# Kernel tuning notes

Hardware: AMD Instinct MI355X
Metric: run time of the kernel (lower is better)

The kernel has to match this reference:

```python
import jax, jax.numpy as jnp
import numpy as np

D_MODEL = 1024
NUM_HEADS = 16
DEPTH = D_MODEL // NUM_HEADS
NEG_BIG = -1e9


def setup_inputs() -> dict:
    key = jax.random.key(0)
    ks = jax.random.split(key, 12)
    B, S = 2, 2048
    scale = 1.0 / np.sqrt(D_MODEL)
    inp = {
        "v": jax.random.normal(ks[0], (B, S, D_MODEL), jnp.float32),
        "k": jax.random.normal(ks[1], (B, S, D_MODEL), jnp.float32),
        "q": jax.random.normal(ks[2], (B, S, D_MODEL), jnp.float32),
        "mask": jnp.zeros((B, 1, 1, S), jnp.float32),
        "Wq": jax.random.normal(ks[3], (D_MODEL, D_MODEL), jnp.float32) * scale,
        "bq": jnp.zeros((D_MODEL,), jnp.float32),
        "Wk": jax.random.normal(ks[4], (D_MODEL, D_MODEL), jnp.float32) * scale,
        "bk": jnp.zeros((D_MODEL,), jnp.float32),
        "Wv": jax.random.normal(ks[5], (D_MODEL, D_MODEL), jnp.float32) * scale,
        "bv": jnp.zeros((D_MODEL,), jnp.float32),
        "Wo": jax.random.normal(ks[6], (D_MODEL, D_MODEL), jnp.float32) * scale,
        "bo": jnp.zeros((D_MODEL,), jnp.float32),
    }
    return inp


def _split_heads(x):
    # (B, S, D) -> (B, H, S, depth)
    B, S, _ = x.shape
    return x.reshape(B, S, NUM_HEADS, DEPTH).transpose(0, 2, 1, 3)


def reference(v, k, q, mask, Wq, bq, Wk, bk, Wv, bv, Wo, bo):
    B, S, _ = q.shape
    qh = _split_heads(q @ Wq + bq)  # (B,H,Sq,depth)
    kh = _split_heads(k @ Wk + bk)  # (B,H,Sk,depth)
    vh = _split_heads(v @ Wv + bv)  # (B,H,Sk,depth)

    logits = jnp.einsum("bhqd,bhkd->bhqk", qh, kh) / jnp.sqrt(
        jnp.asarray(DEPTH, jnp.float32))
    logits = logits + mask * NEG_BIG  # mask broadcasts over heads/queries
    attn = jax.nn.softmax(logits, axis=-1)  # (B,H,Sq,Sk)
    ctx = jnp.einsum("bhqk,bhkd->bhqd", attn, vh)
    ctx = ctx.transpose(0, 2, 1, 3).reshape(B, S, D_MODEL)
    out = ctx @ Wo + bo
    return out, attn
```

## Files before the change

### kernel.cpp

```cpp
#include <hip/hip_runtime.h>
#include <stdint.h>

#define S_LEN 2048
#define DMODEL 1024
#define NHEAD 16
#define DHEAD 64
#define NBATCH 2
#define NE 4194304
#define WN 1048576

typedef unsigned short u16;
typedef float f32x16 __attribute__((ext_vector_type(16)));
typedef __bf16 bf16x8 __attribute__((ext_vector_type(8)));

__device__ __forceinline__ u16 f2bf(float x) {
  union { float f; unsigned u; } v; v.f = x;
  unsigned r = v.u + 0x7fffu + ((v.u >> 16) & 1u);
  return (u16)(r >> 16);
}
__device__ __forceinline__ unsigned cvt_pk_bf16(float lo, float hi) {
  unsigned r;
  asm("v_cvt_pk_bf16_f32 %0, %1, %2" : "=v"(r) : "v"(lo), "v"(hi));
  return r;
}
__device__ __forceinline__ void gld_lds16(const void* g, void* l) {
  __builtin_amdgcn_global_load_lds(
      (const __attribute__((address_space(1))) unsigned*)g,
      (__attribute__((address_space(3))) unsigned*)l, 16, 0, 0);
}

__global__ __launch_bounds__(256) void cvt_inputs(
    const float* __restrict__ q, const float* __restrict__ k, const float* __restrict__ v,
    u16* __restrict__ xq, u16* __restrict__ xk, u16* __restrict__ xv)
{
  int i = blockIdx.x * 256 + threadIdx.x;
  const int stride = gridDim.x * 256;
  for (; i < NE / 4; i += stride) {
    float4 a = ((const float4*)q)[i];
    float4 b = ((const float4*)k)[i];
    float4 c = ((const float4*)v)[i];
    ushort4 oa, ob, oc;
    oa.x = f2bf(a.x); oa.y = f2bf(a.y); oa.z = f2bf(a.z); oa.w = f2bf(a.w);
    ob.x = f2bf(b.x); ob.y = f2bf(b.y); ob.z = f2bf(b.z); ob.w = f2bf(b.w);
    oc.x = f2bf(c.x); oc.y = f2bf(c.y); oc.z = f2bf(c.z); oc.w = f2bf(c.w);
    ((ushort4*)xq)[i] = oa;
    ((ushort4*)xk)[i] = ob;
    ((ushort4*)xv)[i] = oc;
  }
}

__global__ __launch_bounds__(256) void wtrans(
    const float* __restrict__ Wq, const float* __restrict__ Wk,
    const float* __restrict__ Wv, const float* __restrict__ Wo,
    u16* __restrict__ oq, u16* __restrict__ ok, u16* __restrict__ ov, u16* __restrict__ oo)
{
  __shared__ u16 t[64][65];
  const float* W; u16* O;
  if (blockIdx.z == 0)      { W = Wq; O = oq; }
  else if (blockIdx.z == 1) { W = Wk; O = ok; }
  else if (blockIdx.z == 2) { W = Wv; O = ov; }
  else                      { W = Wo; O = oo; }
  const int tid = threadIdx.x;
  const int r0 = blockIdx.y * 64, c0 = blockIdx.x * 64;
#pragma unroll
  for (int i = 0; i < 4; ++i) {
    const int row = i * 16 + (tid >> 4);
    const int col = (tid & 15) * 4;
    float4 wv = *(const float4*)(W + (size_t)(r0 + row) * DMODEL + c0 + col);
    t[row][col + 0] = f2bf(wv.x);
    t[row][col + 1] = f2bf(wv.y);
    t[row][col + 2] = f2bf(wv.z);
    t[row][col + 3] = f2bf(wv.w);
  }
  __syncthreads();
#pragma unroll
  for (int i = 0; i < 4; ++i) {
    const int row = i * 16 + (tid >> 4);
    const int col = (tid & 15) * 4;
    ushort4 o;
    o.x = t[col + 0][row]; o.y = t[col + 1][row];
    o.z = t[col + 2][row]; o.w = t[col + 3][row];
    *(ushort4*)(O + (size_t)(c0 + row) * DMODEL + r0 + col) = o;
  }
}

template <int OUTMODE>
__device__ __forceinline__ void gemm_core(
    const u16* __restrict__ A, const u16* __restrict__ Bt,
    const float* __restrict__ bias, void* __restrict__ outp,
    float scale, int m0, int n0)
{
  __shared__ u16 As[128 * 32];
  __shared__ u16 Bs[128 * 32];
  const int tid = threadIdx.x;
  const int lane = tid & 63, w = tid >> 6;
  const int q_l = lane & 31, hi = lane >> 5;
  const int wr = w >> 1, wc = w & 1;

  f32x16 acc[2][2];
#pragma unroll
  for (int a = 0; a < 2; ++a)
#pragma unroll
    for (int b = 0; b < 2; ++b)
#pragma unroll
      for (int r = 0; r < 16; ++r) acc[a][b][r] = 0.f;

  const u16* srcA = A + (size_t)(m0 + (tid >> 2)) * DMODEL + (tid & 3) * 8;
  const u16* srcB = Bt + (size_t)(n0 + (tid >> 2)) * DMODEL + (tid & 3) * 8;
  u16* dstA = As + w * 512;
  u16* dstB = Bs + w * 512;

  for (int kt = 0; kt < DMODEL; kt += 32) {
    gld_lds16(srcA + kt, dstA);
    gld_lds16(srcA + kt + (size_t)64 * DMODEL, dstA + 2048);
    gld_lds16(srcB + kt, dstB);
    gld_lds16(srcB + kt + (size_t)64 * DMODEL, dstB + 2048);
    __syncthreads();
#pragma unroll
    for (int kk = 0; kk < 2; ++kk) {
      bf16x8 af[2], bfv[2];
#pragma unroll
      for (int mb = 0; mb < 2; ++mb)
        af[mb] = *reinterpret_cast<const bf16x8*>(&As[(wr * 64 + mb * 32 + q_l) * 32 + kk * 16 + hi * 8]);
#pragma unroll
      for (int nb = 0; nb < 2; ++nb)
        bfv[nb] = *reinterpret_cast<const bf16x8*>(&Bs[(wc * 64 + nb * 32 + q_l) * 32 + kk * 16 + hi * 8]);
#pragma unroll
      for (int mb = 0; mb < 2; ++mb)
#pragma unroll
        for (int nb = 0; nb < 2; ++nb)
          acc[mb][nb] = __builtin_amdgcn_mfma_f32_32x32x16_bf16(af[mb], bfv[nb], acc[mb][nb], 0, 0, 0);
    }
    __syncthreads();
  }

#pragma unroll
  for (int mb = 0; mb < 2; ++mb) {
#pragma unroll
    for (int nb = 0; nb < 2; ++nb) {
      const int n = n0 + wc * 64 + nb * 32 + q_l;
      const float bn = bias[n];
#pragma unroll
      for (int r = 0; r < 16; ++r) {
        const int m = m0 + wr * 64 + mb * 32 + (r & 3) + 8 * (r >> 2) + 4 * hi;
        const float val = (acc[mb][nb][r] + bn) * scale;
        if (OUTMODE == 0) {
          const int bb = m >> 11, s = m & 2047, hh = n >> 6, d = n & 63;
          ((u16*)outp)[(((size_t)(bb * NHEAD + hh)) * S_LEN + s) * DHEAD + d] = f2bf(val);
        } else {
          ((float*)outp)[(size_t)m * DMODEL + n] = val;
        }
      }
    }
  }
}

__global__ __launch_bounds__(256) void gemm_qkv(
    const u16* __restrict__ xq, const u16* __restrict__ xk, const u16* __restrict__ xv,
    const u16* __restrict__ wqt, const u16* __restrict__ wkt, const u16* __restrict__ wvt,
    const float* __restrict__ bq, const float* __restrict__ bk, const float* __restrict__ bv,
    u16* __restrict__ qh, u16* __restrict__ kh, u16* __restrict__ vh)
{
  const u16 *A, *Bt; const float* bias; u16* O; float scale;
  if (blockIdx.z == 0)      { A = xq; Bt = wqt; bias = bq; O = qh; scale = 0.125f; }
  else if (blockIdx.z == 1) { A = xk; Bt = wkt; bias = bk; O = kh; scale = 1.f; }
  else                      { A = xv; Bt = wvt; bias = bv; O = vh; scale = 1.f; }
  gemm_core<0>(A, Bt, bias, O, scale, blockIdx.y * 128, blockIdx.x * 128);
}

__global__ __launch_bounds__(256) void vtrans(const u16* __restrict__ vh, u16* __restrict__ vt)
{
  __shared__ u16 t[64][72];
  const int tid = threadIdx.x;
  const int id = blockIdx.x;
  const int h = ((id & 7) << 1) | ((id >> 3) & 1);
  const int b = (id >> 4) & 1;
  const int bh = b * 16 + h;
  const int s0 = (id >> 5) * 64;
  const u16* src = vh + (size_t)bh * S_LEN * DHEAD;
  u16* dst = vt + (size_t)bh * DHEAD * S_LEN;
#pragma unroll
  for (int i = 0; i < 2; ++i) {
    const int row = i * 32 + (tid >> 3);
    const int c8 = (tid & 7) * 8;
    *(uint4*)&t[row][c8] = *(const uint4*)(src + (size_t)(s0 + row) * DHEAD + c8);
  }
  __syncthreads();
#pragma unroll
  for (int i = 0; i < 2; ++i) {
    const int d = i * 32 + (tid >> 3);
    const int c8 = (tid & 7) * 8;
    unsigned p0 = (unsigned)t[c8 + 0][d] | ((unsigned)t[c8 + 1][d] << 16);
    unsigned p1 = (unsigned)t[c8 + 2][d] | ((unsigned)t[c8 + 3][d] << 16);
    unsigned p2 = (unsigned)t[c8 + 4][d] | ((unsigned)t[c8 + 5][d] << 16);
    unsigned p3 = (unsigned)t[c8 + 6][d] | ((unsigned)t[c8 + 7][d] << 16);
    uint4 o; o.x = p0; o.y = p1; o.z = p2; o.w = p3;
    *(uint4*)(dst + (size_t)d * S_LEN + s0 + c8) = o;
  }
}

__global__ __launch_bounds__(64) void attn_pv(
    const u16* __restrict__ qh, const u16* __restrict__ kh,
    const u16* __restrict__ vt, const float* __restrict__ mask,
    float* __restrict__ inv_g, u16* __restrict__ ctx_out)
{
  const int lane = threadIdx.x;
  const int q_l = lane & 31, hi = lane >> 5;
  const int id = blockIdx.x;
  const int h = ((id & 7) << 1) | ((id >> 3) & 1);
  const int b = (id >> 4) & 1;
  const int bh = b * 16 + h;
  const int qb = id >> 5;
  const int q0 = qb * 32;

  const u16* Qp = qh + (size_t)bh * S_LEN * DHEAD;
  const u16* Kp = kh + (size_t)bh * S_LEN * DHEAD;
  const u16* Vp = vt + (size_t)bh * DHEAD * S_LEN;
  const float* mrow = mask + (size_t)b * S_LEN;

  bf16x8 qf[4];
  {
    const u16* qrow = Qp + (size_t)(q0 + q_l) * DHEAD + hi * 8;
#pragma unroll
    for (int c = 0; c < 4; ++c) qf[c] = *reinterpret_cast<const bf16x8*>(qrow + c * 16);
  }

  float rsum = 0.f;
  f32x16 cacc[2];
#pragma unroll
  for (int db = 0; db < 2; ++db)
#pragma unroll
    for (int r = 0; r < 16; ++r) cacc[db][r] = 0.f;

  bf16x8 kc[4], kn[4], vc[2][2], vn[2][2];
  {
    const u16* kr0 = Kp + (size_t)q_l * DHEAD + hi * 8;
#pragma unroll
    for (int c = 0; c < 4; ++c) kc[c] = *reinterpret_cast<const bf16x8*>(kr0 + c * 16);
#pragma unroll
    for (int s2 = 0; s2 < 2; ++s2)
#pragma unroll
      for (int db = 0; db < 2; ++db)
        vc[s2][db] = *reinterpret_cast<const bf16x8*>(
            Vp + (size_t)(db * 32 + q_l) * S_LEN + s2 * 16 + hi * 8);
  }

#pragma unroll 2
  for (int t = 0; t < 64; ++t) {
    const int k0 = t * 32;
    if (t < 63) {
      const u16* krow = Kp + (size_t)(k0 + 32 + q_l) * DHEAD + hi * 8;
#pragma unroll
      for (int c = 0; c < 4; ++c) kn[c] = *reinterpret_cast<const bf16x8*>(krow + c * 16);
#pragma unroll
      for (int s2 = 0; s2 < 2; ++s2)
#pragma unroll
        for (int db = 0; db < 2; ++db)
          vn[s2][db] = *reinterpret_cast<const bf16x8*>(
              Vp + (size_t)(db * 32 + q_l) * S_LEN + k0 + 32 + s2 * 16 + hi * 8);
    }
    f32x16 a0, a1;
#pragma unroll
    for (int r = 0; r < 16; ++r) { a0[r] = 0.f; a1[r] = 0.f; }
    a0 = __builtin_amdgcn_mfma_f32_32x32x16_bf16(kc[0], qf[0], a0, 0, 0, 0);
    a0 = __builtin_amdgcn_mfma_f32_32x32x16_bf16(kc[1], qf[1], a0, 0, 0, 0);
    a1 = __builtin_amdgcn_mfma_f32_32x32x16_bf16(kc[2], qf[2], a1, 0, 0, 0);
    a1 = __builtin_amdgcn_mfma_f32_32x32x16_bf16(kc[3], qf[3], a1, 0, 0, 0);

    float p[16];
#pragma unroll
    for (int g = 0; g < 4; ++g) {
      const float4 mk = *(const float4*)&mrow[k0 + 8 * g + 4 * hi];
      p[4 * g + 0] = __expf(a0[4 * g + 0] + a1[4 * g + 0] + mk.x * -1e9f);
      p[4 * g + 1] = __expf(a0[4 * g + 1] + a1[4 * g + 1] + mk.y * -1e9f);
      p[4 * g + 2] = __expf(a0[4 * g + 2] + a1[4 * g + 2] + mk.z * -1e9f);
      p[4 * g + 3] = __expf(a0[4 * g + 3] + a1[4 * g + 3] + mk.w * -1e9f);
      rsum += (p[4 * g + 0] + p[4 * g + 1]) + (p[4 * g + 2] + p[4 * g + 3]);
    }
    unsigned pk[8];
#pragma unroll
    for (int g = 0; g < 4; ++g) {
      pk[2 * g + 0] = cvt_pk_bf16(p[4 * g + 0], p[4 * g + 1]);
      pk[2 * g + 1] = cvt_pk_bf16(p[4 * g + 2], p[4 * g + 3]);
    }
#pragma unroll
    for (int s2 = 0; s2 < 2; ++s2) {
      unsigned a0u = pk[4 * s2 + 0], b0u = pk[4 * s2 + 2];
      unsigned a1u = pk[4 * s2 + 1], b1u = pk[4 * s2 + 3];
      asm volatile("v_permlane32_swap_b32 %0, %1" : "+v"(a0u), "+v"(b0u));
      asm volatile("v_permlane32_swap_b32 %0, %1" : "+v"(a1u), "+v"(b1u));
      uint4 frw; frw.x = a0u; frw.y = a1u; frw.z = b0u; frw.w = b1u;
      bf16x8 pa = __builtin_bit_cast(bf16x8, frw);
#pragma unroll
      for (int db = 0; db < 2; ++db)
        cacc[db] = __builtin_amdgcn_mfma_f32_32x32x16_bf16(pa, vc[s2][db], cacc[db], 0, 0, 0);
    }
#pragma unroll
    for (int c = 0; c < 4; ++c) kc[c] = kn[c];
#pragma unroll
    for (int s2 = 0; s2 < 2; ++s2)
#pragma unroll
      for (int db = 0; db < 2; ++db) vc[s2][db] = vn[s2][db];
  }

  rsum += __shfl_xor(rsum, 32, 64);
  const float inv = 1.0f / rsum;
  if (lane < 32) inv_g[(size_t)bh * S_LEN + q0 + lane] = inv;

  float sc[16];
#pragma unroll
  for (int r = 0; r < 16; ++r)
    sc[r] = __shfl(inv, (r & 3) + 8 * (r >> 2) + 4 * hi, 64);
#pragma unroll
  for (int db = 0; db < 2; ++db)
#pragma unroll
    for (int r = 0; r < 16; ++r) {
      const int qq = (r & 3) + 8 * (r >> 2) + 4 * hi;
      ctx_out[((size_t)(b * S_LEN + q0 + qq)) * DMODEL + h * DHEAD + db * 32 + q_l] =
          f2bf(cacc[db][r] * sc[r]);
    }
}

__global__ __launch_bounds__(256) void tail_fused(
    const u16* __restrict__ ctx, const u16* __restrict__ wot, const float* __restrict__ bo,
    float* __restrict__ out,
    const u16* __restrict__ qh, const u16* __restrict__ kh,
    const float* __restrict__ mask, const float* __restrict__ inv_g,
    float* __restrict__ attn_out)
{
  if (blockIdx.x < 256) {
    const int gid = blockIdx.x;
    gemm_core<1>(ctx, wot, bo, out, 1.f, (gid >> 3) * 128, (gid & 7) * 128);
    return;
  }
  const int id = blockIdx.x - 256;
  const int tid = threadIdx.x;
  const int lane = tid & 63, w = tid >> 6;
  const int q_l = lane & 31, hi = lane >> 5;
  const int h = ((id & 7) << 1) | ((id >> 3) & 1);
  const int b = (id >> 4) & 1;
  const int bh = b * 16 + h;
  const int qb = id >> 5;
  const int q0 = qb * 32;

  const u16* Qp = qh + (size_t)bh * S_LEN * DHEAD;
  const u16* Kp = kh + (size_t)bh * S_LEN * DHEAD;

  bf16x8 qf[4];
  {
    const u16* qrow = Qp + (size_t)(q0 + q_l) * DHEAD + hi * 8;
#pragma unroll
    for (int c = 0; c < 4; ++c) qf[c] = *reinterpret_cast<const bf16x8*>(qrow + c * 16);
  }

  float myinv[16];
#pragma unroll
  for (int r = 0; r < 16; ++r)
    myinv[r] = inv_g[(size_t)bh * S_LEN + q0 + (r & 3) + 8 * (r >> 2) + 4 * hi];

  const int k0w = w * 512;
  float mval[16];
#pragma unroll
  for (int t = 0; t < 16; ++t)
    mval[t] = mask[(size_t)b * S_LEN + k0w + t * 32 + q_l] * -1e9f;

  float* base = attn_out + ((size_t)bh * S_LEN + q0 + 4 * hi) * S_LEN + k0w + q_l;

  bf16x8 kc[4], kn[4];
  {
    const u16* kr0 = Kp + (size_t)(k0w + q_l) * DHEAD + hi * 8;
#pragma unroll
    for (int c = 0; c < 4; ++c) kc[c] = *reinterpret_cast<const bf16x8*>(kr0 + c * 16);
  }

#pragma unroll
  for (int t = 0; t < 16; ++t) {
    if (t < 15) {
      const u16* krow = Kp + (size_t)(k0w + (t + 1) * 32 + q_l) * DHEAD + hi * 8;
#pragma unroll
      for (int c = 0; c < 4; ++c) kn[c] = *reinterpret_cast<const bf16x8*>(krow + c * 16);
    }
    f32x16 a0, a1;
#pragma unroll
    for (int r = 0; r < 16; ++r) { a0[r] = 0.f; a1[r] = 0.f; }
    a0 = __builtin_amdgcn_mfma_f32_32x32x16_bf16(qf[0], kc[0], a0, 0, 0, 0);
    a0 = __builtin_amdgcn_mfma_f32_32x32x16_bf16(qf[1], kc[1], a0, 0, 0, 0);
    a1 = __builtin_amdgcn_mfma_f32_32x32x16_bf16(qf[2], kc[2], a1, 0, 0, 0);
    a1 = __builtin_amdgcn_mfma_f32_32x32x16_bf16(qf[3], kc[3], a1, 0, 0, 0);
#pragma unroll
    for (int r = 0; r < 16; ++r) {
      const float pv = __expf(a0[r] + a1[r] + mval[t]) * myinv[r];
      const int rr = (r & 3) + 8 * (r >> 2);
      __builtin_nontemporal_store(pv, &base[(size_t)rr * S_LEN + t * 32]);
    }
#pragma unroll
    for (int c = 0; c < 4; ++c) kc[c] = kn[c];
  }
}

extern "C" void kernel_launch(void* const* d_in, const int* in_sizes, int n_in,
                              void* d_out, int out_size, void* d_ws, size_t ws_size,
                              hipStream_t stream)
{
  (void)in_sizes; (void)n_in; (void)out_size; (void)ws_size;
  const float* v    = (const float*)d_in[0];
  const float* k    = (const float*)d_in[1];
  const float* q    = (const float*)d_in[2];
  const float* mask = (const float*)d_in[3];
  const float* Wq   = (const float*)d_in[4];
  const float* bq   = (const float*)d_in[5];
  const float* Wk   = (const float*)d_in[6];
  const float* bk   = (const float*)d_in[7];
  const float* Wv   = (const float*)d_in[8];
  const float* bv   = (const float*)d_in[9];
  const float* Wo   = (const float*)d_in[10];
  const float* bo   = (const float*)d_in[11];

  u16* ws16 = (u16*)d_ws;
  u16* xq  = ws16;
  u16* xk  = ws16 + (size_t)1 * NE;
  u16* xv  = ws16 + (size_t)2 * NE;
  u16* qh  = ws16 + (size_t)3 * NE;
  u16* kh  = ws16 + (size_t)4 * NE;
  u16* vh  = ws16 + (size_t)5 * NE;
  u16* wqt = ws16 + (size_t)6 * NE;
  u16* wkt = wqt + WN;
  u16* wvt = wkt + WN;
  u16* wot = wvt + WN;
  float* inv_g = (float*)(wot + WN);
  u16* vt  = xq;
  u16* ctx = xk;

  float* outp  = (float*)d_out;
  float* attnp = outp + (size_t)NE;

  cvt_inputs<<<dim3(1024), dim3(256), 0, stream>>>(q, k, v, xq, xk, xv);
  wtrans<<<dim3(16, 16, 4), dim3(256), 0, stream>>>(Wq, Wk, Wv, Wo, wqt, wkt, wvt, wot);
  gemm_qkv<<<dim3(8, 32, 3), dim3(256), 0, stream>>>(xq, xk, xv, wqt, wkt, wvt,
                                                     bq, bk, bv, qh, kh, vh);
  vtrans<<<dim3(1024), dim3(256), 0, stream>>>(vh, vt);
  attn_pv<<<dim3(2048), dim3(64), 0, stream>>>(qh, kh, vt, mask, inv_g, ctx);
  tail_fused<<<dim3(2304), dim3(256), 0, stream>>>(ctx, wot, bo, outp,
                                                   qh, kh, mask, inv_g, attnp);
}
```

Before: 314.1 us.

## Run PV and attention-probability writing concurrently in one kernel, split output GEMM

Merges the PV/context computation and the attention-matrix writer into one launch with 2560 blocks, so the memory-bound attn write overlaps the compute-bound PV pass. The attn writer no longer waits on a global inv_g buffer; instead each block recomputes the row sums itself across 4 waves and reduces them in shared memory. The output projection GEMM moves to its own kernel after the mega kernel. The cost is a redundant QK^T and exp pass for the row sums in the writer blocks, plus the PV path now packs 4 waves per block.

```diff
diff --git a/kernel.cpp b/kernel.cpp
--- a/kernel.cpp
+++ b/kernel.cpp
@@ -168,6 +168,13 @@
   gemm_core<0>(A, Bt, bias, O, scale, blockIdx.y * 128, blockIdx.x * 128);
 }
 
+__global__ __launch_bounds__(256) void gemm_out(
+    const u16* __restrict__ ctx, const u16* __restrict__ wot,
+    const float* __restrict__ bo, float* __restrict__ out)
+{
+  gemm_core<1>(ctx, wot, bo, out, 1.f, blockIdx.y * 128, blockIdx.x * 128);
+}
+
 __global__ __launch_bounds__(256) void vtrans(const u16* __restrict__ vh, u16* __restrict__ vt)
 {
   __shared__ u16 t[64][72];
@@ -199,23 +206,142 @@
   }
 }
 
-__global__ __launch_bounds__(64) void attn_pv(
+__global__ __launch_bounds__(256) void attn_mega(
     const u16* __restrict__ qh, const u16* __restrict__ kh,
     const u16* __restrict__ vt, const float* __restrict__ mask,
-    float* __restrict__ inv_g, u16* __restrict__ ctx_out)
-{
-  const int lane = threadIdx.x;
+    u16* __restrict__ ctx_out, float* __restrict__ attn_out)
+{
+  const int tid = threadIdx.x;
+  const int lane = tid & 63, w = tid >> 6;
   const int q_l = lane & 31, hi = lane >> 5;
-  const int id = blockIdx.x;
+
+  if (blockIdx.x < 512) {
+    const int ib = blockIdx.x;
+    const int x = ib & 7;
+    const int j = ((ib >> 3) << 2) + w;
+    const int h = (x << 1) | (j & 1);
+    const int b = (j >> 1) & 1;
+    const int bh = b * 16 + h;
+    const int q0 = (j >> 2) * 32;
+
+    const u16* Qp = qh + (size_t)bh * S_LEN * DHEAD;
+    const u16* Kp = kh + (size_t)bh * S_LEN * DHEAD;
+    const u16* Vp = vt + (size_t)bh * DHEAD * S_LEN;
+    const float* mrow = mask + (size_t)b * S_LEN;
+
+    bf16x8 qf[4];
+    {
+      const u16* qrow = Qp + (size_t)(q0 + q_l) * DHEAD + hi * 8;
+#pragma unroll
+      for (int c = 0; c < 4; ++c) qf[c] = *reinterpret_cast<const bf16x8*>(qrow + c * 16);
+    }
+
+    float rsum = 0.f;
+    f32x16 cacc[2];
+#pragma unroll
+    for (int db = 0; db < 2; ++db)
+#pragma unroll
+      for (int r = 0; r < 16; ++r) cacc[db][r] = 0.f;
+
+    bf16x8 kc[4], kn[4], vc[2][2], vn[2][2];
+    {
+      const u16* kr0 = Kp + (size_t)q_l * DHEAD + hi * 8;
+#pragma unroll
+      for (int c = 0; c < 4; ++c) kc[c] = *reinterpret_cast<const bf16x8*>(kr0 + c * 16);
+#pragma unroll
+      for (int s2 = 0; s2 < 2; ++s2)
+#pragma unroll
+        for (int db = 0; db < 2; ++db)
+          vc[s2][db] = *reinterpret_cast<const bf16x8*>(
+              Vp + (size_t)(db * 32 + q_l) * S_LEN + s2 * 16 + hi * 8);
+    }
+
+#pragma unroll 2
+    for (int t = 0; t < 64; ++t) {
+      const int k0 = t * 32;
+      if (t < 63) {
+        const u16* krow = Kp + (size_t)(k0 + 32 + q_l) * DHEAD + hi * 8;
+#pragma unroll
+        for (int c = 0; c < 4; ++c) kn[c] = *reinterpret_cast<const bf16x8*>(krow + c * 16);
+#pragma unroll
+        for (int s2 = 0; s2 < 2; ++s2)
+#pragma unroll
+          for (int db = 0; db < 2; ++db)
+            vn[s2][db] = *reinterpret_cast<const bf16x8*>(
+                Vp + (size_t)(db * 32 + q_l) * S_LEN + k0 + 32 + s2 * 16 + hi * 8);
+      }
+      f32x16 a0, a1;
+#pragma unroll
+      for (int r = 0; r < 16; ++r) { a0[r] = 0.f; a1[r] = 0.f; }
+      a0 = __builtin_amdgcn_mfma_f32_32x32x16_bf16(kc[0], qf[0], a0, 0, 0, 0);
+      a0 = __builtin_amdgcn_mfma_f32_32x32x16_bf16(kc[1], qf[1], a0, 0, 0, 0);
+      a1 = __builtin_amdgcn_mfma_f32_32x32x16_bf16(kc[2], qf[2], a1, 0, 0, 0);
+      a1 = __builtin_amdgcn_mfma_f32_32x32x16_bf16(kc[3], qf[3], a1, 0, 0, 0);
+
+      float p[16];
+#pragma unroll
+      for (int g = 0; g < 4; ++g) {
+        const float4 mk = *(const float4*)&mrow[k0 + 8 * g + 4 * hi];
+        p[4 * g + 0] = __expf(a0[4 * g + 0] + a1[4 * g + 0] + mk.x * -1e9f);
+        p[4 * g + 1] = __expf(a0[4 * g + 1] + a1[4 * g + 1] + mk.y * -1e9f);
+        p[4 * g + 2] = __expf(a0[4 * g + 2] + a1[4 * g + 2] + mk.z * -1e9f);
+        p[4 * g + 3] = __expf(a0[4 * g + 3] + a1[4 * g + 3] + mk.w * -1e9f);
+        rsum += (p[4 * g + 0] + p[4 * g + 1]) + (p[4 * g + 2] + p[4 * g + 3]);
+      }
+      unsigned pk[8];
+#pragma unroll
+      for (int g = 0; g < 4; ++g) {
+        pk[2 * g + 0] = cvt_pk_bf16(p[4 * g + 0], p[4 * g + 1]);
+        pk[2 * g + 1] = cvt_pk_bf16(p[4 * g + 2], p[4 * g + 3]);
+      }
+#pragma unroll
+      for (int s2 = 0; s2 < 2; ++s2) {
+        unsigned a0u = pk[4 * s2 + 0], b0u = pk[4 * s2 + 2];
+        unsigned a1u = pk[4 * s2 + 1], b1u = pk[4 * s2 + 3];
+        asm volatile("v_permlane32_swap_b32 %0, %1" : "+v"(a0u), "+v"(b0u));
+        asm volatile("v_permlane32_swap_b32 %0, %1" : "+v"(a1u), "+v"(b1u));
+        uint4 frw; frw.x = a0u; frw.y = a1u; frw.z = b0u; frw.w = b1u;
+        bf16x8 pa = __builtin_bit_cast(bf16x8, frw);
+#pragma unroll
+        for (int db = 0; db < 2; ++db)
+          cacc[db] = __builtin_amdgcn_mfma_f32_32x32x16_bf16(pa, vc[s2][db], cacc[db], 0, 0, 0);
+      }
+#pragma unroll
+      for (int c = 0; c < 4; ++c) kc[c] = kn[c];
+#pragma unroll
+      for (int s2 = 0; s2 < 2; ++s2)
+#pragma unroll
+        for (int db = 0; db < 2; ++db) vc[s2][db] = vn[s2][db];
+    }
+
+    rsum += __shfl_xor(rsum, 32, 64);
+    const float inv = 1.0f / rsum;
+    float sc[16];
+#pragma unroll
+    for (int r = 0; r < 16; ++r)
+      sc[r] = __shfl(inv, (r & 3) + 8 * (r >> 2) + 4 * hi, 64);
+#pragma unroll
+    for (int db = 0; db < 2; ++db)
+#pragma unroll
+      for (int r = 0; r < 16; ++r) {
+        const int qq = (r & 3) + 8 * (r >> 2) + 4 * hi;
+        ctx_out[((size_t)(b * S_LEN + q0 + qq)) * DMODEL + h * DHEAD + db * 32 + q_l] =
+            f2bf(cacc[db][r] * sc[r]);
+      }
+    return;
+  }
+
+  __shared__ float srow[4][32];
+  __shared__ float sinv[32];
+  const int id = blockIdx.x - 512;
   const int h = ((id & 7) << 1) | ((id >> 3) & 1);
   const int b = (id >> 4) & 1;
   const int bh = b * 16 + h;
-  const int qb = id >> 5;
-  const int q0 = qb * 32;
+  const int q0 = (id >> 5) * 32;
+  const int k0w = w * 512;
 
   const u16* Qp = qh + (size_t)bh * S_LEN * DHEAD;
   const u16* Kp = kh + (size_t)bh * S_LEN * DHEAD;
-  const u16* Vp = vt + (size_t)bh * DHEAD * S_LEN;
   const float* mrow = mask + (size_t)b * S_LEN;
 
   bf16x8 qf[4];
@@ -226,143 +352,54 @@
   }
 
   float rsum = 0.f;
-  f32x16 cacc[2];
-#pragma unroll
-  for (int db = 0; db < 2; ++db)
-#pragma unroll
-    for (int r = 0; r < 16; ++r) cacc[db][r] = 0.f;
-
-  bf16x8 kc[4], kn[4], vc[2][2], vn[2][2];
   {
-    const u16* kr0 = Kp + (size_t)q_l * DHEAD + hi * 8;
+    bf16x8 kc[4], kn[4];
+    const u16* kr0 = Kp + (size_t)(k0w + q_l) * DHEAD + hi * 8;
 #pragma unroll
     for (int c = 0; c < 4; ++c) kc[c] = *reinterpret_cast<const bf16x8*>(kr0 + c * 16);
 #pragma unroll
-    for (int s2 = 0; s2 < 2; ++s2)
-#pragma unroll
-      for (int db = 0; db < 2; ++db)
-        vc[s2][db] = *reinterpret_cast<const bf16x8*>(
-            Vp + (size_t)(db * 32 + q_l) * S_LEN + s2 * 16 + hi * 8);
-  }
-
-#pragma unroll 2
-  for (int t = 0; t < 64; ++t) {
-    const int k0 = t * 32;
-    if (t < 63) {
-      const u16* krow = Kp + (size_t)(k0 + 32 + q_l) * DHEAD + hi * 8;
-#pragma unroll
-      for (int c = 0; c < 4; ++c) kn[c] = *reinterpret_cast<const bf16x8*>(krow + c * 16);
-#pragma unroll
-      for (int s2 = 0; s2 < 2; ++s2)
-#pragma unroll
-        for (int db = 0; db < 2; ++db)
-          vn[s2][db] = *reinterpret_cast<const bf16x8*>(
-              Vp + (size_t)(db * 32 + q_l) * S_LEN + k0 + 32 + s2 * 16 + hi * 8);
-    }
-    f32x16 a0, a1;
-#pragma unroll
-    for (int r = 0; r < 16; ++r) { a0[r] = 0.f; a1[r] = 0.f; }
-    a0 = __builtin_amdgcn_mfma_f32_32x32x16_bf16(kc[0], qf[0], a0, 0, 0, 0);
-    a0 = __builtin_amdgcn_mfma_f32_32x32x16_bf16(kc[1], qf[1], a0, 0, 0, 0);
-    a1 = __builtin_amdgcn_mfma_f32_32x32x16_bf16(kc[2], qf[2], a1, 0, 0, 0);
-    a1 = __builtin_amdgcn_mfma_f32_32x32x16_bf16(kc[3], qf[3], a1, 0, 0, 0);
-
-    float p[16];
-#pragma unroll
-    for (int g = 0; g < 4; ++g) {
-      const float4 mk = *(const float4*)&mrow[k0 + 8 * g + 4 * hi];
-      p[4 * g + 0] = __expf(a0[4 * g + 0] + a1[4 * g + 0] + mk.x * -1e9f);
-      p[4 * g + 1] = __expf(a0[4 * g + 1] + a1[4 * g + 1] + mk.y * -1e9f);
-      p[4 * g + 2] = __expf(a0[4 * g + 2] + a1[4 * g + 2] + mk.z * -1e9f);
-      p[4 * g + 3] = __expf(a0[4 * g + 3] + a1[4 * g + 3] + mk.w * -1e9f);
-      rsum += (p[4 * g + 0] + p[4 * g + 1]) + (p[4 * g + 2] + p[4 * g + 3]);
-    }
-    unsigned pk[8];
-#pragma unroll
-    for (int g = 0; g < 4; ++g) {
-      pk[2 * g + 0] = cvt_pk_bf16(p[4 * g + 0], p[4 * g + 1]);
-      pk[2 * g + 1] = cvt_pk_bf16(p[4 * g + 2], p[4 * g + 3]);
-    }
-#pragma unroll
-    for (int s2 = 0; s2 < 2; ++s2) {
-      unsigned a0u = pk[4 * s2 + 0], b0u = pk[4 * s2 + 2];
-      unsigned a1u = pk[4 * s2 + 1], b1u = pk[4 * s2 + 3];
-      asm volatile("v_permlane32_swap_b32 %0, %1" : "+v"(a0u), "+v"(b0u));
-      asm volatile("v_permlane32_swap_b32 %0, %1" : "+v"(a1u), "+v"(b1u));
-      uint4 frw; frw.x = a0u; frw.y = a1u; frw.z = b0u; frw.w = b1u;
-      bf16x8 pa = __builtin_bit_cast(bf16x8, frw);
-#pragma unroll
-      for (int db = 0; db < 2; ++db)
-        cacc[db] = __builtin_amdgcn_mfma_f32_32x32x16_bf16(pa, vc[s2][db], cacc[db], 0, 0, 0);
-    }
-#pragma unroll
-    for (int c = 0; c < 4; ++c) kc[c] = kn[c];
-#pragma unroll
-    for (int s2 = 0; s2 < 2; ++s2)
-#pragma unroll
-      for (int db = 0; db < 2; ++db) vc[s2][db] = vn[s2][db];
-  }
-
+    for (int t = 0; t < 16; ++t) {
+      const int k0 = k0w + t * 32;
+      if (t < 15) {
+        const u16* krow = Kp + (size_t)(k0 + 32 + q_l) * DHEAD + hi * 8;
+#pragma unroll
+        for (int c = 0; c < 4; ++c) kn[c] = *reinterpret_cast<const bf16x8*>(krow + c * 16);
+      }
+      f32x16 a0, a1;
+#pragma unroll
+      for (int r = 0; r < 16; ++r) { a0[r] = 0.f; a1[r] = 0.f; }
+      a0 = __builtin_amdgcn_mfma_f32_32x32x16_bf16(kc[0], qf[0], a0, 0, 0, 0);
+      a0 = __builtin_amdgcn_mfma_f32_32x32x16_bf16(kc[1], qf[1], a0, 0, 0, 0);
+      a1 = __builtin_amdgcn_mfma_f32_32x32x16_bf16(kc[2], qf[2], a1, 0, 0, 0);
+      a1 = __builtin_amdgcn_mfma_f32_32x32x16_bf16(kc[3], qf[3], a1, 0, 0, 0);
+#pragma unroll
+      for (int g = 0; g < 4; ++g) {
+        const float4 mk = *(const float4*)&mrow[k0 + 8 * g + 4 * hi];
+        rsum += __expf(a0[4 * g + 0] + a1[4 * g + 0] + mk.x * -1e9f)
+              + __expf(a0[4 * g + 1] + a1[4 * g + 1] + mk.y * -1e9f)
+              + __expf(a0[4 * g + 2] + a1[4 * g + 2] + mk.z * -1e9f)
+              + __expf(a0[4 * g + 3] + a1[4 * g + 3] + mk.w * -1e9f);
+      }
+#pragma unroll
+      for (int c = 0; c < 4; ++c) kc[c] = kn[c];
+    }
+  }
   rsum += __shfl_xor(rsum, 32, 64);
-  const float inv = 1.0f / rsum;
-  if (lane < 32) inv_g[(size_t)bh * S_LEN + q0 + lane] = inv;
-
-  float sc[16];
+  if (lane < 32) srow[w][q_l] = rsum;
+  __syncthreads();
+  if (tid < 32)
+    sinv[tid] = 1.0f / (srow[0][tid] + srow[1][tid] + srow[2][tid] + srow[3][tid]);
+  __syncthreads();
+
+  float myinv[16];
 #pragma unroll
   for (int r = 0; r < 16; ++r)
-    sc[r] = __shfl(inv, (r & 3) + 8 * (r >> 2) + 4 * hi, 64);
-#pragma unroll
-  for (int db = 0; db < 2; ++db)
-#pragma unroll
-    for (int r = 0; r < 16; ++r) {
-      const int qq = (r & 3) + 8 * (r >> 2) + 4 * hi;
-      ctx_out[((size_t)(b * S_LEN + q0 + qq)) * DMODEL + h * DHEAD + db * 32 + q_l] =
-          f2bf(cacc[db][r] * sc[r]);
-    }
-}
-
-__global__ __launch_bounds__(256) void tail_fused(
-    const u16* __restrict__ ctx, const u16* __restrict__ wot, const float* __restrict__ bo,
-    float* __restrict__ out,
-    const u16* __restrict__ qh, const u16* __restrict__ kh,
-    const float* __restrict__ mask, const float* __restrict__ inv_g,
-    float* __restrict__ attn_out)
-{
-  if (blockIdx.x < 256) {
-    const int gid = blockIdx.x;
-    gemm_core<1>(ctx, wot, bo, out, 1.f, (gid >> 3) * 128, (gid & 7) * 128);
-    return;
-  }
-  const int id = blockIdx.x - 256;
-  const int tid = threadIdx.x;
-  const int lane = tid & 63, w = tid >> 6;
-  const int q_l = lane & 31, hi = lane >> 5;
-  const int h = ((id & 7) << 1) | ((id >> 3) & 1);
-  const int b = (id >> 4) & 1;
-  const int bh = b * 16 + h;
-  const int qb = id >> 5;
-  const int q0 = qb * 32;
-
-  const u16* Qp = qh + (size_t)bh * S_LEN * DHEAD;
-  const u16* Kp = kh + (size_t)bh * S_LEN * DHEAD;
-
-  bf16x8 qf[4];
-  {
-    const u16* qrow = Qp + (size_t)(q0 + q_l) * DHEAD + hi * 8;
-#pragma unroll
-    for (int c = 0; c < 4; ++c) qf[c] = *reinterpret_cast<const bf16x8*>(qrow + c * 16);
-  }
-
-  float myinv[16];
-#pragma unroll
-  for (int r = 0; r < 16; ++r)
-    myinv[r] = inv_g[(size_t)bh * S_LEN + q0 + (r & 3) + 8 * (r >> 2) + 4 * hi];
-
-  const int k0w = w * 512;
+    myinv[r] = sinv[(r & 3) + 8 * (r >> 2) + 4 * hi];
+
   float mval[16];
 #pragma unroll
   for (int t = 0; t < 16; ++t)
-    mval[t] = mask[(size_t)b * S_LEN + k0w + t * 32 + q_l] * -1e9f;
+    mval[t] = mrow[k0w + t * 32 + q_l] * -1e9f;
 
   float* base = attn_out + ((size_t)bh * S_LEN + q0 + 4 * hi) * S_LEN + k0w + q_l;
 
@@ -427,7 +464,6 @@
   u16* wkt = wqt + WN;
   u16* wvt = wkt + WN;
   u16* wot = wvt + WN;
-  float* inv_g = (float*)(wot + WN);
   u16* vt  = xq;
   u16* ctx = xk;
 
@@ -439,7 +475,6 @@
   gemm_qkv<<<dim3(8, 32, 3), dim3(256), 0, stream>>>(xq, xk, xv, wqt, wkt, wvt,
                                                      bq, bk, bv, qh, kh, vh);
   vtrans<<<dim3(1024), dim3(256), 0, stream>>>(vh, vt);
-  attn_pv<<<dim3(2048), dim3(64), 0, stream>>>(qh, kh, vt, mask, inv_g, ctx);
-  tail_fused<<<dim3(2304), dim3(256), 0, stream>>>(ctx, wot, bo, outp,
-                                                   qh, kh, mask, inv_g, attnp);
-}
+  attn_mega<<<dim3(2560), dim3(256), 0, stream>>>(qh, kh, vt, mask, ctx, attnp);
+  gemm_out<<<dim3(8, 32), dim3(256), 0, stream>>>(ctx, wot, bo, outp);
+}
```

After: 379.3 us. 1.21x slower.

## Split attention key loop across two waves with shared-memory reduction

Applied to the files above, without the earlier changes.

The attention kernel now runs two wavefronts per block, each covering half of the key sequence (32 tiles instead of 64). Partial row sums and context accumulators go to shared memory, are added after a barrier, normalized, and written as vectorized 16-element bf16 stores. This is meant to halve the serial loop length per wave and add parallelism. In exchange it adds LDS use (about 16KB per block), a sync and a reduction step.

```diff
diff --git a/kernel.cpp b/kernel.cpp
--- a/kernel.cpp
+++ b/kernel.cpp
@@ -199,12 +199,16 @@
   }
 }
 
-__global__ __launch_bounds__(64) void attn_pv(
+__global__ __launch_bounds__(128) void attn_pv(
     const u16* __restrict__ qh, const u16* __restrict__ kh,
     const u16* __restrict__ vt, const float* __restrict__ mask,
     float* __restrict__ inv_g, u16* __restrict__ ctx_out)
 {
-  const int lane = threadIdx.x;
+  __shared__ float sred[2][32][64];
+  __shared__ float srow[2][32];
+
+  const int tid = threadIdx.x;
+  const int lane = tid & 63, w = tid >> 6;
   const int q_l = lane & 31, hi = lane >> 5;
   const int id = blockIdx.x;
   const int h = ((id & 7) << 1) | ((id >> 3) & 1);
@@ -232,9 +236,11 @@
 #pragma unroll
     for (int r = 0; r < 16; ++r) cacc[db][r] = 0.f;
 
+  const int tb = w * 32;
+
   bf16x8 kc[4], kn[4], vc[2][2], vn[2][2];
   {
-    const u16* kr0 = Kp + (size_t)q_l * DHEAD + hi * 8;
+    const u16* kr0 = Kp + (size_t)(tb * 32 + q_l) * DHEAD + hi * 8;
 #pragma unroll
     for (int c = 0; c < 4; ++c) kc[c] = *reinterpret_cast<const bf16x8*>(kr0 + c * 16);
 #pragma unroll
@@ -242,13 +248,13 @@
 #pragma unroll
       for (int db = 0; db < 2; ++db)
         vc[s2][db] = *reinterpret_cast<const bf16x8*>(
-            Vp + (size_t)(db * 32 + q_l) * S_LEN + s2 * 16 + hi * 8);
+            Vp + (size_t)(db * 32 + q_l) * S_LEN + tb * 32 + s2 * 16 + hi * 8);
   }
 
 #pragma unroll 2
-  for (int t = 0; t < 64; ++t) {
-    const int k0 = t * 32;
-    if (t < 63) {
+  for (int t = 0; t < 32; ++t) {
+    const int k0 = (tb + t) * 32;
+    if (t < 31) {
       const u16* krow = Kp + (size_t)(k0 + 32 + q_l) * DHEAD + hi * 8;
 #pragma unroll
       for (int c = 0; c < 4; ++c) kn[c] = *reinterpret_cast<const bf16x8*>(krow + c * 16);
@@ -304,21 +310,31 @@
   }
 
   rsum += __shfl_xor(rsum, 32, 64);
-  const float inv = 1.0f / rsum;
-  if (lane < 32) inv_g[(size_t)bh * S_LEN + q0 + lane] = inv;
-
-  float sc[16];
-#pragma unroll
-  for (int r = 0; r < 16; ++r)
-    sc[r] = __shfl(inv, (r & 3) + 8 * (r >> 2) + 4 * hi, 64);
+  if (lane < 32) srow[w][lane] = rsum;
 #pragma unroll
   for (int db = 0; db < 2; ++db)
 #pragma unroll
     for (int r = 0; r < 16; ++r) {
       const int qq = (r & 3) + 8 * (r >> 2) + 4 * hi;
-      ctx_out[((size_t)(b * S_LEN + q0 + qq)) * DMODEL + h * DHEAD + db * 32 + q_l] =
-          f2bf(cacc[db][r] * sc[r]);
-    }
+      sred[w][qq][db * 32 + q_l] = cacc[db][r];
+    }
+  __syncthreads();
+
+  if (tid < 32)
+    inv_g[(size_t)bh * S_LEN + q0 + tid] = 1.0f / (srow[0][tid] + srow[1][tid]);
+
+  {
+    const int row = tid >> 2;
+    const int d0 = (tid & 3) * 16;
+    const float inv = 1.0f / (srow[0][row] + srow[1][row]);
+    union { u16 us[16]; uint4 v[2]; } ou;
+#pragma unroll
+    for (int j = 0; j < 16; ++j)
+      ou.us[j] = f2bf((sred[0][row][d0 + j] + sred[1][row][d0 + j]) * inv);
+    u16* base = ctx_out + ((size_t)(b * S_LEN + q0 + row)) * DMODEL + h * DHEAD + d0;
+    *(uint4*)base = ou.v[0];
+    *(uint4*)(base + 8) = ou.v[1];
+  }
 }
 
 __global__ __launch_bounds__(256) void tail_fused(
@@ -439,7 +455,7 @@
   gemm_qkv<<<dim3(8, 32, 3), dim3(256), 0, stream>>>(xq, xk, xv, wqt, wkt, wvt,
                                                      bq, bk, bv, qh, kh, vh);
   vtrans<<<dim3(1024), dim3(256), 0, stream>>>(vh, vt);
-  attn_pv<<<dim3(2048), dim3(64), 0, stream>>>(qh, kh, vt, mask, inv_g, ctx);
+  attn_pv<<<dim3(2048), dim3(128), 0, stream>>>(qh, kh, vt, mask, inv_g, ctx);
   tail_fused<<<dim3(2304), dim3(256), 0, stream>>>(ctx, wot, bo, outp,
                                                    qh, kh, mask, inv_g, attnp);
 }
```

Result: no change. 316.0 us (+0.6%).

## Process two 32-query tiles per block to reuse K/V loads

Applied to the files above, without the earlier changes.

Each attn_pv and tail_fused block now handles 64 queries as two 32-row sub-tiles that share the same K and V fragment loads, halving grid sizes. This cuts global/L2 traffic for K and V per query and amortises the loop and mask overhead. In exchange it raises register pressure (double accumulators and Q fragments), lowers the unroll to 1, and leaves fewer blocks, which reduces occupancy and parallelism.

```diff
diff --git a/kernel.cpp b/kernel.cpp
--- a/kernel.cpp
+++ b/kernel.cpp
@@ -199,7 +199,7 @@
   }
 }
 
-__global__ __launch_bounds__(64) void attn_pv(
+__global__ __launch_bounds__(64, 2) void attn_pv(
     const u16* __restrict__ qh, const u16* __restrict__ kh,
     const u16* __restrict__ vt, const float* __restrict__ mask,
     float* __restrict__ inv_g, u16* __restrict__ ctx_out)
@@ -211,26 +211,30 @@
   const int b = (id >> 4) & 1;
   const int bh = b * 16 + h;
   const int qb = id >> 5;
-  const int q0 = qb * 32;
+  const int q0 = qb * 64;
 
   const u16* Qp = qh + (size_t)bh * S_LEN * DHEAD;
   const u16* Kp = kh + (size_t)bh * S_LEN * DHEAD;
   const u16* Vp = vt + (size_t)bh * DHEAD * S_LEN;
   const float* mrow = mask + (size_t)b * S_LEN;
 
-  bf16x8 qf[4];
+  bf16x8 qfA[4], qfB[4];
   {
-    const u16* qrow = Qp + (size_t)(q0 + q_l) * DHEAD + hi * 8;
-#pragma unroll
-    for (int c = 0; c < 4; ++c) qf[c] = *reinterpret_cast<const bf16x8*>(qrow + c * 16);
-  }
-
-  float rsum = 0.f;
-  f32x16 cacc[2];
+    const u16* qrA = Qp + (size_t)(q0 + q_l) * DHEAD + hi * 8;
+    const u16* qrB = Qp + (size_t)(q0 + 32 + q_l) * DHEAD + hi * 8;
+#pragma unroll
+    for (int c = 0; c < 4; ++c) {
+      qfA[c] = *reinterpret_cast<const bf16x8*>(qrA + c * 16);
+      qfB[c] = *reinterpret_cast<const bf16x8*>(qrB + c * 16);
+    }
+  }
+
+  float rsumA = 0.f, rsumB = 0.f;
+  f32x16 caccA[2], caccB[2];
 #pragma unroll
   for (int db = 0; db < 2; ++db)
 #pragma unroll
-    for (int r = 0; r < 16; ++r) cacc[db][r] = 0.f;
+    for (int r = 0; r < 16; ++r) { caccA[db][r] = 0.f; caccB[db][r] = 0.f; }
 
   bf16x8 kc[4], kn[4], vc[2][2], vn[2][2];
   {
@@ -245,7 +249,7 @@
             Vp + (size_t)(db * 32 + q_l) * S_LEN + s2 * 16 + hi * 8);
   }
 
-#pragma unroll 2
+#pragma unroll 1
   for (int t = 0; t < 64; ++t) {
     const int k0 = t * 32;
     if (t < 63) {
@@ -259,41 +263,79 @@
           vn[s2][db] = *reinterpret_cast<const bf16x8*>(
               Vp + (size_t)(db * 32 + q_l) * S_LEN + k0 + 32 + s2 * 16 + hi * 8);
     }
-    f32x16 a0, a1;
-#pragma unroll
-    for (int r = 0; r < 16; ++r) { a0[r] = 0.f; a1[r] = 0.f; }
-    a0 = __builtin_amdgcn_mfma_f32_32x32x16_bf16(kc[0], qf[0], a0, 0, 0, 0);
-    a0 = __builtin_amdgcn_mfma_f32_32x32x16_bf16(kc[1], qf[1], a0, 0, 0, 0);
-    a1 = __builtin_amdgcn_mfma_f32_32x32x16_bf16(kc[2], qf[2], a1, 0, 0, 0);
-    a1 = __builtin_amdgcn_mfma_f32_32x32x16_bf16(kc[3], qf[3], a1, 0, 0, 0);
-
-    float p[16];
-#pragma unroll
-    for (int g = 0; g < 4; ++g) {
-      const float4 mk = *(const float4*)&mrow[k0 + 8 * g + 4 * hi];
-      p[4 * g + 0] = __expf(a0[4 * g + 0] + a1[4 * g + 0] + mk.x * -1e9f);
-      p[4 * g + 1] = __expf(a0[4 * g + 1] + a1[4 * g + 1] + mk.y * -1e9f);
-      p[4 * g + 2] = __expf(a0[4 * g + 2] + a1[4 * g + 2] + mk.z * -1e9f);
-      p[4 * g + 3] = __expf(a0[4 * g + 3] + a1[4 * g + 3] + mk.w * -1e9f);
-      rsum += (p[4 * g + 0] + p[4 * g + 1]) + (p[4 * g + 2] + p[4 * g + 3]);
-    }
-    unsigned pk[8];
-#pragma unroll
-    for (int g = 0; g < 4; ++g) {
-      pk[2 * g + 0] = cvt_pk_bf16(p[4 * g + 0], p[4 * g + 1]);
-      pk[2 * g + 1] = cvt_pk_bf16(p[4 * g + 2], p[4 * g + 3]);
-    }
-#pragma unroll
-    for (int s2 = 0; s2 < 2; ++s2) {
-      unsigned a0u = pk[4 * s2 + 0], b0u = pk[4 * s2 + 2];
-      unsigned a1u = pk[4 * s2 + 1], b1u = pk[4 * s2 + 3];
-      asm volatile("v_permlane32_swap_b32 %0, %1" : "+v"(a0u), "+v"(b0u));
-      asm volatile("v_permlane32_swap_b32 %0, %1" : "+v"(a1u), "+v"(b1u));
-      uint4 frw; frw.x = a0u; frw.y = a1u; frw.z = b0u; frw.w = b1u;
-      bf16x8 pa = __builtin_bit_cast(bf16x8, frw);
-#pragma unroll
-      for (int db = 0; db < 2; ++db)
-        cacc[db] = __builtin_amdgcn_mfma_f32_32x32x16_bf16(pa, vc[s2][db], cacc[db], 0, 0, 0);
+    {
+      f32x16 a0, a1;
+#pragma unroll
+      for (int r = 0; r < 16; ++r) { a0[r] = 0.f; a1[r] = 0.f; }
+      a0 = __builtin_amdgcn_mfma_f32_32x32x16_bf16(kc[0], qfA[0], a0, 0, 0, 0);
+      a0 = __builtin_amdgcn_mfma_f32_32x32x16_bf16(kc[1], qfA[1], a0, 0, 0, 0);
+      a1 = __builtin_amdgcn_mfma_f32_32x32x16_bf16(kc[2], qfA[2], a1, 0, 0, 0);
+      a1 = __builtin_amdgcn_mfma_f32_32x32x16_bf16(kc[3], qfA[3], a1, 0, 0, 0);
+      float p[16];
+#pragma unroll
+      for (int g = 0; g < 4; ++g) {
+        const float4 mk = *(const float4*)&mrow[k0 + 8 * g + 4 * hi];
+        p[4 * g + 0] = __expf(a0[4 * g + 0] + a1[4 * g + 0] + mk.x * -1e9f);
+        p[4 * g + 1] = __expf(a0[4 * g + 1] + a1[4 * g + 1] + mk.y * -1e9f);
+        p[4 * g + 2] = __expf(a0[4 * g + 2] + a1[4 * g + 2] + mk.z * -1e9f);
+        p[4 * g + 3] = __expf(a0[4 * g + 3] + a1[4 * g + 3] + mk.w * -1e9f);
+        rsumA += (p[4 * g + 0] + p[4 * g + 1]) + (p[4 * g + 2] + p[4 * g + 3]);
+      }
+      unsigned pk[8];
+#pragma unroll
+      for (int g = 0; g < 4; ++g) {
+        pk[2 * g + 0] = cvt_pk_bf16(p[4 * g + 0], p[4 * g + 1]);
+        pk[2 * g + 1] = cvt_pk_bf16(p[4 * g + 2], p[4 * g + 3]);
+      }
+#pragma unroll
+      for (int s2 = 0; s2 < 2; ++s2) {
+        unsigned x0 = pk[4 * s2 + 0], y0 = pk[4 * s2 + 2];
+        unsigned x1 = pk[4 * s2 + 1], y1 = pk[4 * s2 + 3];
+        asm volatile("v_permlane32_swap_b32 %0, %1" : "+v"(x0), "+v"(y0));
+        asm volatile("v_permlane32_swap_b32 %0, %1" : "+v"(x1), "+v"(y1));
+        uint4 fr; fr.x = x0; fr.y = x1; fr.z = y0; fr.w = y1;
+        bf16x8 pa = __builtin_bit_cast(bf16x8, fr);
+#pragma unroll
+        for (int db = 0; db < 2; ++db)
+          caccA[db] = __builtin_amdgcn_mfma_f32_32x32x16_bf16(pa, vc[s2][db], caccA[db], 0, 0, 0);
+      }
+    }
+    {
+      f32x16 a0, a1;
+#pragma unroll
+      for (int r = 0; r < 16; ++r) { a0[r] = 0.f; a1[r] = 0.f; }
+      a0 = __builtin_amdgcn_mfma_f32_32x32x16_bf16(kc[0], qfB[0], a0, 0, 0, 0);
+      a0 = __builtin_amdgcn_mfma_f32_32x32x16_bf16(kc[1], qfB[1], a0, 0, 0, 0);
+      a1 = __builtin_amdgcn_mfma_f32_32x32x16_bf16(kc[2], qfB[2], a1, 0, 0, 0);
+      a1 = __builtin_amdgcn_mfma_f32_32x32x16_bf16(kc[3], qfB[3], a1, 0, 0, 0);
+      float p[16];
+#pragma unroll
+      for (int g = 0; g < 4; ++g) {
+        const float4 mk = *(const float4*)&mrow[k0 + 8 * g + 4 * hi];
+        p[4 * g + 0] = __expf(a0[4 * g + 0] + a1[4 * g + 0] + mk.x * -1e9f);
+        p[4 * g + 1] = __expf(a0[4 * g + 1] + a1[4 * g + 1] + mk.y * -1e9f);
+        p[4 * g + 2] = __expf(a0[4 * g + 2] + a1[4 * g + 2] + mk.z * -1e9f);
+        p[4 * g + 3] = __expf(a0[4 * g + 3] + a1[4 * g + 3] + mk.w * -1e9f);
+        rsumB += (p[4 * g + 0] + p[4 * g + 1]) + (p[4 * g + 2] + p[4 * g + 3]);
+      }
+      unsigned pk[8];
+#pragma unroll
+      for (int g = 0; g < 4; ++g) {
+        pk[2 * g + 0] = cvt_pk_bf16(p[4 * g + 0], p[4 * g + 1]);
+        pk[2 * g + 1] = cvt_pk_bf16(p[4 * g + 2], p[4 * g + 3]);
+      }
+#pragma unroll
+      for (int s2 = 0; s2 < 2; ++s2) {
+        unsigned x0 = pk[4 * s2 + 0], y0 = pk[4 * s2 + 2];
+        unsigned x1 = pk[4 * s2 + 1], y1 = pk[4 * s2 + 3];
+        asm volatile("v_permlane32_swap_b32 %0, %1" : "+v"(x0), "+v"(y0));
+        asm volatile("v_permlane32_swap_b32 %0, %1" : "+v"(x1), "+v"(y1));
+        uint4 fr; fr.x = x0; fr.y = x1; fr.z = y0; fr.w = y1;
+        bf16x8 pb = __builtin_bit_cast(bf16x8, fr);
+#pragma unroll
+        for (int db = 0; db < 2; ++db)
+          caccB[db] = __builtin_amdgcn_mfma_f32_32x32x16_bf16(pb, vc[s2][db], caccB[db], 0, 0, 0);
+      }
     }
 #pragma unroll
     for (int c = 0; c < 4; ++c) kc[c] = kn[c];
@@ -303,21 +345,31 @@
       for (int db = 0; db < 2; ++db) vc[s2][db] = vn[s2][db];
   }
 
-  rsum += __shfl_xor(rsum, 32, 64);
-  const float inv = 1.0f / rsum;
-  if (lane < 32) inv_g[(size_t)bh * S_LEN + q0 + lane] = inv;
-
-  float sc[16];
-#pragma unroll
-  for (int r = 0; r < 16; ++r)
-    sc[r] = __shfl(inv, (r & 3) + 8 * (r >> 2) + 4 * hi, 64);
+  rsumA += __shfl_xor(rsumA, 32, 64);
+  rsumB += __shfl_xor(rsumB, 32, 64);
+  const float invA = 1.0f / rsumA;
+  const float invB = 1.0f / rsumB;
+  if (lane < 32) {
+    inv_g[(size_t)bh * S_LEN + q0 + lane] = invA;
+    inv_g[(size_t)bh * S_LEN + q0 + 32 + lane] = invB;
+  }
+
+  float scA[16], scB[16];
+#pragma unroll
+  for (int r = 0; r < 16; ++r) {
+    const int src = (r & 3) + 8 * (r >> 2) + 4 * hi;
+    scA[r] = __shfl(invA, src, 64);
+    scB[r] = __shfl(invB, src, 64);
+  }
 #pragma unroll
   for (int db = 0; db < 2; ++db)
 #pragma unroll
     for (int r = 0; r < 16; ++r) {
       const int qq = (r & 3) + 8 * (r >> 2) + 4 * hi;
       ctx_out[((size_t)(b * S_LEN + q0 + qq)) * DMODEL + h * DHEAD + db * 32 + q_l] =
-          f2bf(cacc[db][r] * sc[r]);
+          f2bf(caccA[db][r] * scA[r]);
+      ctx_out[((size_t)(b * S_LEN + q0 + 32 + qq)) * DMODEL + h * DHEAD + db * 32 + q_l] =
+          f2bf(caccB[db][r] * scB[r]);
     }
 }
 
@@ -341,22 +393,29 @@
   const int b = (id >> 4) & 1;
   const int bh = b * 16 + h;
   const int qb = id >> 5;
-  const int q0 = qb * 32;
+  const int q0 = qb * 64;
 
   const u16* Qp = qh + (size_t)bh * S_LEN * DHEAD;
   const u16* Kp = kh + (size_t)bh * S_LEN * DHEAD;
 
-  bf16x8 qf[4];
+  bf16x8 qfA[4], qfB[4];
   {
-    const u16* qrow = Qp + (size_t)(q0 + q_l) * DHEAD + hi * 8;
-#pragma unroll
-    for (int c = 0; c < 4; ++c) qf[c] = *reinterpret_cast<const bf16x8*>(qrow + c * 16);
-  }
-
-  float myinv[16];
-#pragma unroll
-  for (int r = 0; r < 16; ++r)
-    myinv[r] = inv_g[(size_t)bh * S_LEN + q0 + (r & 3) + 8 * (r >> 2) + 4 * hi];
+    const u16* qrA = Qp + (size_t)(q0 + q_l) * DHEAD + hi * 8;
+    const u16* qrB = Qp + (size_t)(q0 + 32 + q_l) * DHEAD + hi * 8;
+#pragma unroll
+    for (int c = 0; c < 4; ++c) {
+      qfA[c] = *reinterpret_cast<const bf16x8*>(qrA + c * 16);
+      qfB[c] = *reinterpret_cast<const bf16x8*>(qrB + c * 16);
+    }
+  }
+
+  float myinvA[16], myinvB[16];
+#pragma unroll
+  for (int r = 0; r < 16; ++r) {
+    const int rq = (r & 3) + 8 * (r >> 2) + 4 * hi;
+    myinvA[r] = inv_g[(size_t)bh * S_LEN + q0 + rq];
+    myinvB[r] = inv_g[(size_t)bh * S_LEN + q0 + 32 + rq];
+  }
 
   const int k0w = w * 512;
   float mval[16];
@@ -364,7 +423,8 @@
   for (int t = 0; t < 16; ++t)
     mval[t] = mask[(size_t)b * S_LEN + k0w + t * 32 + q_l] * -1e9f;
 
-  float* base = attn_out + ((size_t)bh * S_LEN + q0 + 4 * hi) * S_LEN + k0w + q_l;
+  float* baseA = attn_out + ((size_t)bh * S_LEN + q0 + 4 * hi) * S_LEN + k0w + q_l;
+  float* baseB = attn_out + ((size_t)bh * S_LEN + q0 + 32 + 4 * hi) * S_LEN + k0w + q_l;
 
   bf16x8 kc[4], kn[4];
   {
@@ -380,18 +440,35 @@
 #pragma unroll
       for (int c = 0; c < 4; ++c) kn[c] = *reinterpret_cast<const bf16x8*>(krow + c * 16);
     }
-    f32x16 a0, a1;
-#pragma unroll
-    for (int r = 0; r < 16; ++r) { a0[r] = 0.f; a1[r] = 0.f; }
-    a0 = __builtin_amdgcn_mfma_f32_32x32x16_bf16(qf[0], kc[0], a0, 0, 0, 0);
-    a0 = __builtin_amdgcn_mfma_f32_32x32x16_bf16(qf[1], kc[1], a0, 0, 0, 0);
-    a1 = __builtin_amdgcn_mfma_f32_32x32x16_bf16(qf[2], kc[2], a1, 0, 0, 0);
-    a1 = __builtin_amdgcn_mfma_f32_32x32x16_bf16(qf[3], kc[3], a1, 0, 0, 0);
-#pragma unroll
-    for (int r = 0; r < 16; ++r) {
-      const float pv = __expf(a0[r] + a1[r] + mval[t]) * myinv[r];
-      const int rr = (r & 3) + 8 * (r >> 2);
-      __builtin_nontemporal_store(pv, &base[(size_t)rr * S_LEN + t * 32]);
+    {
+      f32x16 a0, a1;
+#pragma unroll
+      for (int r = 0; r < 16; ++r) { a0[r] = 0.f; a1[r] = 0.f; }
+      a0 = __builtin_amdgcn_mfma_f32_32x32x16_bf16(qfA[0], kc[0], a0, 0, 0, 0);
+      a0 = __builtin_amdgcn_mfma_f32_32x32x16_bf16(qfA[1], kc[1], a0, 0, 0, 0);
+      a1 = __builtin_amdgcn_mfma_f32_32x32x16_bf16(qfA[2], kc[2], a1, 0, 0, 0);
+      a1 = __builtin_amdgcn_mfma_f32_32x32x16_bf16(qfA[3], kc[3], a1, 0, 0, 0);
+#pragma unroll
+      for (int r = 0; r < 16; ++r) {
+        const float pv = __expf(a0[r] + a1[r] + mval[t]) * myinvA[r];
+        const int rr = (r & 3) + 8 * (r >> 2);
+        __builtin_nontemporal_store(pv, &baseA[(size_t)rr * S_LEN + t * 32]);
+      }
+    }
+    {
+      f32x16 a0, a1;
+#pragma unroll
+      for (int r = 0; r < 16; ++r) { a0[r] = 0.f; a1[r] = 0.f; }
+      a0 = __builtin_amdgcn_mfma_f32_32x32x16_bf16(qfB[0], kc[0], a0, 0, 0, 0);
+      a0 = __builtin_amdgcn_mfma_f32_32x32x16_bf16(qfB[1], kc[1], a0, 0, 0, 0);
+      a1 = __builtin_amdgcn_mfma_f32_32x32x16_bf16(qfB[2], kc[2], a1, 0, 0, 0);
+      a1 = __builtin_amdgcn_mfma_f32_32x32x16_bf16(qfB[3], kc[3], a1, 0, 0, 0);
+#pragma unroll
+      for (int r = 0; r < 16; ++r) {
+        const float pv = __expf(a0[r] + a1[r] + mval[t]) * myinvB[r];
+        const int rr = (r & 3) + 8 * (r >> 2);
+        __builtin_nontemporal_store(pv, &baseB[(size_t)rr * S_LEN + t * 32]);
+      }
     }
 #pragma unroll
     for (int c = 0; c < 4; ++c) kc[c] = kn[c];
@@ -439,7 +516,7 @@
   gemm_qkv<<<dim3(8, 32, 3), dim3(256), 0, stream>>>(xq, xk, xv, wqt, wkt, wvt,
                                                      bq, bk, bv, qh, kh, vh);
   vtrans<<<dim3(1024), dim3(256), 0, stream>>>(vh, vt);
-  attn_pv<<<dim3(2048), dim3(64), 0, stream>>>(qh, kh, vt, mask, inv_g, ctx);
-  tail_fused<<<dim3(2304), dim3(256), 0, stream>>>(ctx, wot, bo, outp,
+  attn_pv<<<dim3(1024), dim3(64), 0, stream>>>(qh, kh, vt, mask, inv_g, ctx);
+  tail_fused<<<dim3(1280), dim3(256), 0, stream>>>(ctx, wot, bo, outp,
                                                    qh, kh, mask, inv_g, attnp);
 }
```

New measurement: 299.1 us (median of 2 runs). 1.05x faster.
